# Optimization experiments

Hardware: AMD Instinct MI355X
Metric: run time of the kernel (lower is better)

## Reference

```python
import jax, jax.numpy as jnp
import numpy as np
from jax import lax

FEAT = 192   # features
GROUP = 3
B, H, W = 16, 64, 64
CIN = 2 * FEAT        # 384, input channels of x
CGATE = 4 * FEAT      # 768, gate channels


def _group_ids(C, g=GROUP):
    # contiguous channel blocks: channel c -> group c*g//C
    return (np.arange(C) * g) // C


def _mask_B(out_c, in_c, kw):
    # PixelRNN mask 'B' for a (1,kw) kernel: left-of-center columns fully
    # connected, center column obeys group rule (out_group >= in_group),
    # right-of-center columns blocked.
    og = _group_ids(out_c)[:, None]
    ig = _group_ids(in_c)[None, :]
    center = (og >= ig).astype(np.float32)  # (out_c, in_c)
    m = np.zeros((out_c, in_c, 1, kw), dtype=np.float32)
    m[:, :, :, : kw // 2] = 1.0
    m[:, :, 0, kw // 2] = center
    return jnp.asarray(m)


def _shuffle(h):
    # (B, 3*4*(F/3), H, W): group-major gate layout -> gate-major group layout
    b, c, hh, ww = h.shape
    return h.reshape(b, GROUP, 4, FEAT // GROUP, hh, ww) \
            .transpose(0, 2, 1, 3, 4, 5).reshape(b, c, hh, ww)


def setup_inputs() -> dict:
    key = jax.random.key(0)
    k1, k2, k3, k4, k5 = jax.random.split(key, 5)
    x = jax.random.normal(k1, (B, CIN, H, W), dtype=jnp.float32)
    w_i2s = jax.random.normal(k2, (CGATE, CIN, 1, 3), dtype=jnp.float32) * 0.02
    w_s2s = jax.random.normal(k3, (CGATE, FEAT, 1, 3), dtype=jnp.float32) * 0.02
    w_skip = jax.random.normal(k4, (CIN, FEAT, 1, 1), dtype=jnp.float32) * 0.05
    b_skip = jax.random.normal(k5, (CIN,), dtype=jnp.float32) * 0.01
    return {"x": x, "w_i2s": w_i2s, "w_s2s": w_s2s,
            "w_skip": w_skip, "b_skip": b_skip}


def reference(x, w_i2s, w_s2s, w_skip, b_skip):
    mask_i2s = _mask_B(CGATE, CIN, 3)
    mask_skip = _mask_B(CIN, FEAT, 1)

    # input-to-state: masked (1,3) conv, 'same' padding on width
    h = lax.conv_general_dilated(
        x, w_i2s * mask_i2s, (1, 1), ((0, 0), (1, 1)),
        dimension_numbers=("NCHW", "OIHW", "NCHW"))
    h = _shuffle(h)                       # (B, 4F, H, W)

    w1 = w_s2s[:, :, 0, :]                # (4F, F, 3) for 1D width conv
    h_rows = h.transpose(2, 0, 1, 3)      # (H, B, 4F, W)

    def step(carry, h_row):
        _h, c = carry                     # each (B, F, W)
        s = lax.conv_general_dilated(
            _h, w1, (1,), ((1, 1),),
            dimension_numbers=("NCW", "OIW", "NCW")) + h_row
        o, f, i, g = jnp.split(jax.nn.sigmoid(s), 4, axis=1)
        c = f * c + i * g
        _h = o * jnp.tanh(c)
        return (_h, c), _h

    init = (jnp.zeros((B, FEAT, W), x.dtype), jnp.zeros((B, FEAT, W), x.dtype))
    _, out_h = lax.scan(step, init, h_rows)   # (H, B, F, W)
    out_h = out_h.transpose(1, 2, 0, 3)       # (B, F, H, W)

    skip = lax.conv_general_dilated(
        out_h, w_skip * mask_skip, (1, 1), ((0, 0), (0, 0)),
        dimension_numbers=("NCHW", "OIHW", "NCHW")) + b_skip[None, :, None, None]
    return x + skip
```

## Files before the change

### kernel.cpp

```cpp
#include <hip/hip_runtime.h>
#include <hip/hip_cooperative_groups.h>
#include <cmath>

#define FEAT  192
#define CINCH 384
#define CGATE 768
#define BATCH 16
#define HH    64
#define WW    64
#define NP    (BATCH*HH*WW)
#define KI2S  768
#define KS2S  576
#define NBLK  192
#define SCANT 512

using bf16   = __bf16;
using bf16x8 = __attribute__((ext_vector_type(8))) __bf16;
using bf16x4 = __attribute__((ext_vector_type(4))) __bf16;
using f32x4  = __attribute__((ext_vector_type(4))) float;
typedef unsigned long long u64;

__device__ __forceinline__ void ic_store64(u64* p, u64 v) {
    __hip_atomic_store(p, v, __ATOMIC_RELAXED, __HIP_MEMORY_SCOPE_AGENT);
}
__device__ __forceinline__ u64 ic_load64(const u64* p) {
    return __hip_atomic_load(p, __ATOMIC_RELAXED, __HIP_MEMORY_SCOPE_AGENT);
}
__device__ __forceinline__ void ic_store32(unsigned* p, unsigned v) {
    __hip_atomic_store(p, v, __ATOMIC_RELAXED, __HIP_MEMORY_SCOPE_AGENT);
}
__device__ __forceinline__ unsigned ic_load32(const unsigned* p) {
    return __hip_atomic_load(p, __ATOMIC_RELAXED, __HIP_MEMORY_SCOPE_AGENT);
}
__device__ __forceinline__ void ic_store16(bf16* p, bf16 h) {
    union { bf16 h; unsigned short u; } cv; cv.h = h;
    __hip_atomic_store((unsigned short*)p, cv.u, __ATOMIC_RELAXED, __HIP_MEMORY_SCOPE_AGENT);
}
__device__ __forceinline__ float ic_load_bf16(const bf16* p) {
    union { unsigned short u; bf16 h; } cv;
    cv.u = __hip_atomic_load((const unsigned short*)p, __ATOMIC_RELAXED, __HIP_MEMORY_SCOPE_AGENT);
    return (float)cv.h;
}

__device__ __forceinline__ float sigm_fast(float v) {
    return __builtin_amdgcn_rcpf(1.f + __expf(-v));
}
__device__ __forceinline__ float tanh_fast(float v) {
    return 1.f - 2.f * __builtin_amdgcn_rcpf(1.f + __expf(2.f * v));
}

__global__ void pack_weights(const float* __restrict__ wi, const float* __restrict__ ws,
                             const float* __restrict__ wk,
                             bf16* __restrict__ WpA, bf16* __restrict__ WpS,
                             bf16* __restrict__ WpK, bf16* __restrict__ zp) {
    int tid = blockIdx.x * 256 + threadIdx.x;
    int stride = gridDim.x * 256;
    for (int idx = tid; idx < 512; idx += stride) zp[idx] = (bf16)0.f;
    for (int idx = tid; idx < CGATE * KI2S; idx += stride) {
        int cp = idx / KI2S, k = idx % KI2S;
        int q = cp / 192, r = cp % 192, g = r / 64, f = r % 64;
        int c = g * 256 + q * 64 + f;
        float v;
        if (k < CINCH) {
            v = wi[(c * CINCH + k) * 3 + 0];
        } else {
            int ic = k - CINCH;
            v = (g >= ic / 128) ? wi[(c * CINCH + ic) * 3 + 1] : 0.f;
        }
        WpA[idx] = (bf16)v;
    }
    for (int idx = tid; idx < CGATE * KS2S; idx += stride) {
        int oc = idx / KS2S, k = idx % KS2S;
        int t = k / FEAT, f = k % FEAT;
        WpS[idx] = (bf16)ws[(oc * FEAT + f) * 3 + t];
    }
    for (int idx = tid; idx < CINCH * FEAT; idx += stride) {
        int co = idx / FEAT, f = idx % FEAT;
        WpK[idx] = (co / 128 >= f / 64) ? (bf16)wk[idx] : (bf16)0.f;
    }
}

__global__ void pack_xc(const float* __restrict__ x, bf16* __restrict__ Xc) {
    __shared__ float tile[64][65];
    int b = blockIdx.x >> 6, y = blockIdx.x & 63;
    const float* xb = x + ((size_t)b * CINCH * HH + y) * WW;
    bf16* Xrow = Xc + (size_t)((b * HH + y) * WW) * CINCH;
    for (int ic0 = 0; ic0 < CINCH; ic0 += 64) {
        for (int rep = 0; rep < 16; ++rep) {
            int idx = rep * 256 + threadIdx.x;
            int i = idx >> 6, w = idx & 63;
            tile[i][w] = xb[(size_t)(ic0 + i) * (HH * WW) + w];
        }
        __syncthreads();
        for (int rep = 0; rep < 16; ++rep) {
            int idx = rep * 256 + threadIdx.x;
            int w = idx >> 6, i = idx & 63;
            Xrow[(size_t)w * CINCH + ic0 + i] = (bf16)tile[i][w];
        }
        __syncthreads();
    }
}

__global__ __launch_bounds__(SCANT, 2) void scan_kernel(
    const bf16* __restrict__ WpA,
    const bf16* __restrict__ Ws2s,
    const bf16* __restrict__ Wskip,
    const bf16* __restrict__ Xc,
    const bf16* __restrict__ zp,
    const float* __restrict__ x,
    const float* __restrict__ b_skip,
    float* __restrict__ out,
    bf16* __restrict__ hg,
    unsigned* __restrict__ cnt,
    bf16* __restrict__ Hring) {
    cooperative_groups::grid_group grid = cooperative_groups::this_grid();
    __shared__ __align__(16) bf16 hlds[66 * 200];
    __shared__ __align__(16) bf16 hnew[64 * 20];
    __shared__ __align__(16) bf16 As2[128 * 64];
    __shared__ __align__(16) bf16 Bs2[128 * 64];
    const int bid = blockIdx.x;
    const int b = (bid & 7) * 2 + (bid / 96);
    const int j = (bid >> 3) % 12;
    const int tid = threadIdx.x, lane = tid & 63, wid = tid >> 6;
    const int quad = lane >> 4, col = lane & 15;
    const int wh = wid & 3;
    const int wn = wid >> 2;
    const int mq = wid & 1, nq = wid >> 1;

    {
        const int total = 3 * 16 * 66 * 192 / 2;
        for (int i = bid * SCANT + tid; i < total; i += NBLK * SCANT)
            ((unsigned*)hg)[i] = 0u;
        if (tid < 32) cnt[(bid % 16) * 32 + tid] = 0u;
        if (tid >= 64 && tid < 96) cnt[512 + (bid % 16) * 32 + (tid - 64)] = 0u;
        for (int i = tid; i < 66 * 100; i += SCANT) ((unsigned*)hlds)[i] = 0u;
    }
    bf16x8 Ag[18];
    {
        int f = 16 * j + wh * 4 + (col >> 2), q = col & 3;
        const bf16* Arow = Ws2s + (size_t)(q * 192 + f) * KS2S + quad * 8;
        for (int kc = 0; kc < 18; ++kc) Ag[kc] = *(const bf16x8*)(Arow + kc * 32);
    }
    bf16x8 Ak[6];
    const int mtk = wid & 1, ntk = wid >> 1;
    {
        int co = 32 * j + mtk * 16 + col;
        const bf16* Krow = Wskip + (size_t)co * FEAT + quad * 8;
        for (int kc = 0; kc < 6; ++kc) Ak[kc] = *(const bf16x8*)(Krow + kc * 32);
    }
    const int fmine = 16 * j + wh * 4 + quad;
    const int lf = wh * 4 + quad;
    float cstate[2] = {0.f, 0.f};
    unsigned* myflags = cnt + b * 32;
    unsigned* gflags  = cnt + 512 + b * 32;
    grid.sync();

#define GSTAGE(M0, P0, K0) do {                                                    \
    _Pragma("unroll")                                                              \
    for (int r_ = 0; r_ < 2; ++r_) {                                               \
        int L_ = r_ * 512 + tid;                                                   \
        int row_ = L_ >> 3, slot_ = L_ & 7;                                        \
        int c_ = slot_ ^ (row_ & 7);                                               \
        const bf16* srcA = &WpA[(size_t)((M0) + row_) * KI2S + (K0) + c_ * 8];     \
        const bf16* srcB;                                                          \
        if ((K0) < 384) {                                                          \
            srcB = ((row_ & 63) == 0) ? (zp + c_ * 8)                              \
                 : &Xc[(size_t)((P0) + row_ - 1) * CINCH + (K0) + c_ * 8];         \
        } else {                                                                   \
            srcB = &Xc[(size_t)((P0) + row_) * CINCH + (K0) - 384 + c_ * 8];       \
        }                                                                          \
        bf16* dA = As2 + (size_t)(r_ * 512 + wid * 64) * 8;                        \
        bf16* dB = Bs2 + (size_t)(r_ * 512 + wid * 64) * 8;                        \
        __builtin_amdgcn_global_load_lds(                                          \
            (const __attribute__((address_space(1))) void*)srcA,                   \
            (__attribute__((address_space(3))) void*)dA, 16, 0, 0);                \
        __builtin_amdgcn_global_load_lds(                                          \
            (const __attribute__((address_space(1))) void*)srcB,                   \
            (__attribute__((address_space(3))) void*)dB, 16, 0, 0);                \
    }                                                                              \
} while (0)

#define GMFMA(ACC) do {                                                            \
    _Pragma("unroll")                                                              \
    for (int kk_ = 0; kk_ < 2; ++kk_) {                                            \
        bf16x8 af_[4], bv_[2];                                                     \
        _Pragma("unroll")                                                          \
        for (int mt_ = 0; mt_ < 4; ++mt_) {                                        \
            int row_ = mq * 64 + mt_ * 16 + col;                                   \
            int slot_ = (kk_ * 4 + quad) ^ (row_ & 7);                             \
            af_[mt_] = *(const bf16x8*)(&As2[row_ * 64 + slot_ * 8]);              \
        }                                                                          \
        _Pragma("unroll")                                                          \
        for (int nt_ = 0; nt_ < 2; ++nt_) {                                        \
            int row_ = nq * 32 + nt_ * 16 + col;                                   \
            int slot_ = (kk_ * 4 + quad) ^ (row_ & 7);                             \
            bv_[nt_] = *(const bf16x8*)(&Bs2[row_ * 64 + slot_ * 8]);              \
        }                                                                          \
        _Pragma("unroll")                                                          \
        for (int mt_ = 0; mt_ < 4; ++mt_)                                          \
            _Pragma("unroll")                                                      \
            for (int nt_ = 0; nt_ < 2; ++nt_)                                      \
                ACC[mt_][nt_] = __builtin_amdgcn_mfma_f32_16x16x32_bf16(           \
                    af_[mt_], bv_[nt_], ACC[mt_][nt_], 0, 0, 0);                   \
    }                                                                              \
} while (0)

#define GEPI(ACC, M0, YH) do {                                                     \
    _Pragma("unroll")                                                              \
    for (int mt_ = 0; mt_ < 4; ++mt_)                                              \
        _Pragma("unroll")                                                          \
        for (int nt_ = 0; nt_ < 2; ++nt_) {                                        \
            int m_ = (M0) + mq * 64 + mt_ * 16 + quad * 4;                         \
            int idx_ = nq * 32 + nt_ * 16 + col;                                   \
            int yy_ = (YH) * 2 + (idx_ >> 6), wl_ = idx_ & 63;                     \
            _Pragma("unroll")                                                      \
            for (int r_ = 0; r_ < 4; ++r_)                                         \
                ic_store16(&Hring[(((size_t)(m_ + r_) * 16 + b) * 8 +              \
                                   (yy_ & 7)) * 64 + wl_],                         \
                           (bf16)ACC[mt_][nt_][r_]);                               \
        }                                                                          \
} while (0)

#define HPREF(YY) do {                                                             \
    int slot_ = (YY) & 7;                                                          \
    _Pragma("unroll")                                                              \
    for (int i_ = 0; i_ < 2; ++i_) {                                               \
        int w_ = (wn * 2 + i_) * 16 + col;                                         \
        _Pragma("unroll")                                                          \
        for (int r_ = 0; r_ < 4; ++r_)                                             \
            hadd[i_][r_] = ic_load_bf16(&Hring[(((size_t)(r_ * FEAT + fmine) * 16  \
                                                 + b) * 8 + slot_) * 64 + w_]);    \
    }                                                                              \
} while (0)

    f32x4 accg[4][2];
    float hadd[2][4];

    {
        const int t0 = j;
        const int m0_ = (t0 % 6) * 128, yh_ = t0 / 6;
        const size_t p0_ = ((size_t)b * 64 + yh_ * 2) * 64;
        #pragma unroll
        for (int mt_ = 0; mt_ < 4; ++mt_)
            for (int nt_ = 0; nt_ < 2; ++nt_) accg[mt_][nt_] = f32x4{0.f, 0.f, 0.f, 0.f};
        for (int ki = 0; ki < 12; ++ki) {
            GSTAGE(m0_, p0_, ki * 64);
            __syncthreads();
            GMFMA(accg);
            __syncthreads();
        }
        GEPI(accg, m0_, yh_);
        __syncthreads();
        if (tid == 0) ic_store32(&gflags[j], 1u);
        while (true) {
            unsigned v = (lane < 12) ? ic_load32(&gflags[lane]) : 1u;
            if (__ballot(v >= 1u) == ~0ull) break;
            __builtin_amdgcn_s_sleep(1);
        }
        asm volatile("" ::: "memory");
        HPREF(0);
    }

    for (int y = 0; y < 64; ++y) {
        f32x4 acc[2] = {};
        for (int kc = 0; kc < 18; ++kc) {
            int k0 = kc * 32 + quad * 8;
            int t = k0 / FEAT, f = k0 % FEAT;
            #pragma unroll
            for (int i = 0; i < 2; ++i) {
                int w = (wn * 2 + i) * 16 + col;
                bf16x8 bfr = *(const bf16x8*)(&hlds[(w + t) * 200 + f]);
                acc[i] = __builtin_amdgcn_mfma_f32_16x16x32_bf16(Ag[kc], bfr, acc[i], 0, 0, 0);
            }
        }
        #pragma unroll
        for (int i = 0; i < 2; ++i) {
            int w = (wn * 2 + i) * 16 + col;
            float so = acc[i][0] + hadd[i][0];
            float sf = acc[i][1] + hadd[i][1];
            float si = acc[i][2] + hadd[i][2];
            float sg = acc[i][3] + hadd[i][3];
            float go = sigm_fast(so);
            float gf = sigm_fast(sf);
            float gi = sigm_fast(si);
            float gg = sigm_fast(sg);
            float cc = gf * cstate[i] + gi * gg;
            cstate[i] = cc;
            hnew[w * 20 + lf] = (bf16)(go * tanh_fast(cc));
        }
        __syncthreads();

        if (tid < 256) {
            bf16* dst = hg + ((size_t)(y % 3) * 16 + b) * (66 * 192);
            int w = tid >> 2, fo = (tid & 3) * 4;
            u64 v = *(const u64*)(&hnew[w * 20 + fo]);
            ic_store64((u64*)(dst + (size_t)(w + 1) * 192 + 16 * j + fo), v);
        }
        __syncthreads();
        if (tid == 0) ic_store32(&myflags[j], (unsigned)(y + 1));

        if (y < 60) {
            const int n_ = (y >> 2) + 1;
            const int t_ = j + 12 * n_;
            const int m0_ = (t_ % 6) * 128, yh_ = t_ / 6;
            const size_t p0_ = ((size_t)b * 64 + yh_ * 2) * 64;
            const int ph_ = y & 3;
            if (ph_ == 0) {
                #pragma unroll
                for (int mt_ = 0; mt_ < 4; ++mt_)
                    for (int nt_ = 0; nt_ < 2; ++nt_) accg[mt_][nt_] = f32x4{0.f, 0.f, 0.f, 0.f};
            }
            for (int ki = ph_ * 3; ki < ph_ * 3 + 3; ++ki) {
                GSTAGE(m0_, p0_, ki * 64);
                __syncthreads();
                GMFMA(accg);
                __syncthreads();
            }
            if (ph_ == 3) {
                GEPI(accg, m0_, yh_);
                __syncthreads();
                if (tid == 0) ic_store32(&gflags[j], (unsigned)(n_ + 1));
            }
        }

        if (y < 63) {
            const int yhreq = (y + 1) >> 1;
            unsigned tgt = 0;
            if (lane < 12) {
                int o = (lane >= 6) ? 1 : 0;
                tgt = (yhreq >= o) ? (unsigned)(((yhreq - o) >> 1) + 1) : 0u;
            }
            while (true) {
                unsigned v = (lane < 12) ? ic_load32(&gflags[lane]) : 0u;
                if (__ballot(v >= tgt) == ~0ull) break;
                __builtin_amdgcn_s_sleep(1);
            }
            asm volatile("" ::: "memory");
            HPREF(y + 1);
        }

        if (y > 0) {
            const int ym = y - 1;
            f32x4 acc2 = {};
            int wsk = ntk * 16 + col;
            for (int kc = 0; kc < 6; ++kc) {
                bf16x8 bfr = *(const bf16x8*)(&hlds[(wsk + 1) * 200 + kc * 32 + quad * 8]);
                acc2 = __builtin_amdgcn_mfma_f32_16x16x32_bf16(Ak[kc], bfr, acc2, 0, 0, 0);
            }
            for (int r = 0; r < 4; ++r) {
                int co = 32 * j + mtk * 16 + quad * 4 + r;
                size_t xi = ((size_t)(b * CINCH + co) * HH + ym) * WW + wsk;
                out[xi] = x[xi] + b_skip[co] + acc2[r];
            }
        }
        __syncthreads();

        {
            const unsigned tgt = (unsigned)(y + 1);
            while (true) {
                unsigned v = (lane < 12) ? ic_load32(&myflags[lane]) : tgt;
                if (__ballot(v >= tgt) == ~0ull) break;
                __builtin_amdgcn_s_sleep(1);
            }
            asm volatile("" ::: "memory");
        }

        {
            const u64* src = (const u64*)(hg + ((size_t)(y % 3) * 16 + b) * (66 * 192));
            #pragma unroll
            for (int it = 0; it < 7; ++it) {
                int c = it * SCANT + tid;
                if (c < 66 * 48) {
                    u64 v = ic_load64(src + c);
                    int w = c / 48, fc = c % 48;
                    *(u64*)(&hlds[w * 200 + fc * 4]) = v;
                }
            }
        }
        __syncthreads();
    }

    {
        f32x4 acc2 = {};
        int wsk = ntk * 16 + col;
        for (int kc = 0; kc < 6; ++kc) {
            bf16x8 bfr = *(const bf16x8*)(&hlds[(wsk + 1) * 200 + kc * 32 + quad * 8]);
            acc2 = __builtin_amdgcn_mfma_f32_16x16x32_bf16(Ak[kc], bfr, acc2, 0, 0, 0);
        }
        for (int r = 0; r < 4; ++r) {
            int co = 32 * j + mtk * 16 + quad * 4 + r;
            size_t xi = ((size_t)(b * CINCH + co) * HH + 63) * WW + wsk;
            out[xi] = x[xi] + b_skip[co] + acc2[r];
        }
    }

#undef GSTAGE
#undef GMFMA
#undef GEPI
#undef HPREF
}

extern "C" void kernel_launch(void* const* d_in, const int* in_sizes, int n_in,
                              void* d_out, int out_size, void* d_ws, size_t ws_size,
                              hipStream_t stream) {
    const float* x      = (const float*)d_in[0];
    const float* w_i2s  = (const float*)d_in[1];
    const float* w_s2s  = (const float*)d_in[2];
    const float* w_skip = (const float*)d_in[3];
    const float* b_skip = (const float*)d_in[4];
    float* out = (float*)d_out;

    char* ws = (char*)d_ws;
    bf16* Xc    = (bf16*)ws;
    size_t off  = (size_t)NP * CINCH * 2;
    bf16* WpA   = (bf16*)(ws + off); off += (size_t)CGATE * KI2S * 2;
    bf16* WpS   = (bf16*)(ws + off); off += (size_t)CGATE * KS2S * 2;
    bf16* WpK   = (bf16*)(ws + off); off += (size_t)CINCH * FEAT * 2;
    bf16* hg    = (bf16*)(ws + off); off += (size_t)3 * 16 * 66 * 192 * 2;
    bf16* Hring = (bf16*)(ws + off); off += (size_t)CGATE * 16 * 8 * 64 * 2;
    unsigned* cnt = (unsigned*)(ws + off); off += 4096;
    bf16* zp    = (bf16*)(ws + off); off += 1024;

    pack_weights<<<256, 256, 0, stream>>>(w_i2s, w_s2s, w_skip, WpA, WpS, WpK, zp);
    pack_xc<<<BATCH * HH, 256, 0, stream>>>(x, Xc);

    void* args[] = { (void*)&WpA, (void*)&WpS, (void*)&WpK, (void*)&Xc, (void*)&zp,
                     (void*)&x, (void*)&b_skip, (void*)&out, (void*)&hg, (void*)&cnt,
                     (void*)&Hring };
    hipLaunchCooperativeKernel((const void*)scan_kernel, dim3(NBLK), dim3(SCANT),
                               args, 0, stream);
}
```

Before: 771.7 us.

## Offload input-to-state GEMM to dedicated producer blocks with deeper ring buffer

Adds 64 producer blocks to the cooperative grid. They compute the input-to-state gate GEMM tiles ahead of the recurrent scan, using double-buffered LDS staging, and write the results into a Hring buffer enlarged from 8 to 16 rows. The 192 scan blocks no longer interleave GEMM slices into each recurrence step, which takes that work off the latency-critical scan loop. In exchange the grid needs more co-resident blocks and more LDS per block, and producers must spin on scan progress flags to avoid overrunning the ring.

```diff
diff --git a/kernel.cpp b/kernel.cpp
--- a/kernel.cpp
+++ b/kernel.cpp
@@ -11,8 +11,11 @@
 #define NP    (BATCH*HH*WW)
 #define KI2S  768
 #define KS2S  576
-#define NBLK  192
+#define NSCAN 192
+#define NPROD 64
+#define NBLK  (NSCAN+NPROD)
 #define SCANT 512
+#define RING  16
 
 using bf16   = __bf16;
 using bf16x8 = __attribute__((ext_vector_type(8))) __bf16;
@@ -114,48 +117,29 @@
     unsigned* __restrict__ cnt,
     bf16* __restrict__ Hring) {
     cooperative_groups::grid_group grid = cooperative_groups::this_grid();
-    __shared__ __align__(16) bf16 hlds[66 * 200];
-    __shared__ __align__(16) bf16 hnew[64 * 20];
-    __shared__ __align__(16) bf16 As2[128 * 64];
-    __shared__ __align__(16) bf16 Bs2[128 * 64];
+    __shared__ __align__(16) bf16 smem[32768];
+    bf16* const hlds = smem;
+    bf16* const hnew = smem + 13200;
     const int bid = blockIdx.x;
-    const int b = (bid & 7) * 2 + (bid / 96);
-    const int j = (bid >> 3) % 12;
+    const bool isScan = bid < NSCAN;
     const int tid = threadIdx.x, lane = tid & 63, wid = tid >> 6;
     const int quad = lane >> 4, col = lane & 15;
-    const int wh = wid & 3;
-    const int wn = wid >> 2;
     const int mq = wid & 1, nq = wid >> 1;
 
     {
         const int total = 3 * 16 * 66 * 192 / 2;
         for (int i = bid * SCANT + tid; i < total; i += NBLK * SCANT)
             ((unsigned*)hg)[i] = 0u;
-        if (tid < 32) cnt[(bid % 16) * 32 + tid] = 0u;
-        if (tid >= 64 && tid < 96) cnt[512 + (bid % 16) * 32 + (tid - 64)] = 0u;
-        for (int i = tid; i < 66 * 100; i += SCANT) ((unsigned*)hlds)[i] = 0u;
-    }
-    bf16x8 Ag[18];
-    {
-        int f = 16 * j + wh * 4 + (col >> 2), q = col & 3;
-        const bf16* Arow = Ws2s + (size_t)(q * 192 + f) * KS2S + quad * 8;
-        for (int kc = 0; kc < 18; ++kc) Ag[kc] = *(const bf16x8*)(Arow + kc * 32);
-    }
-    bf16x8 Ak[6];
-    const int mtk = wid & 1, ntk = wid >> 1;
-    {
-        int co = 32 * j + mtk * 16 + col;
-        const bf16* Krow = Wskip + (size_t)co * FEAT + quad * 8;
-        for (int kc = 0; kc < 6; ++kc) Ak[kc] = *(const bf16x8*)(Krow + kc * 32);
-    }
-    const int fmine = 16 * j + wh * 4 + quad;
-    const int lf = wh * 4 + quad;
-    float cstate[2] = {0.f, 0.f};
-    unsigned* myflags = cnt + b * 32;
-    unsigned* gflags  = cnt + 512 + b * 32;
+        if (isScan) {
+            if (tid < 32) cnt[(bid % 16) * 32 + tid] = 0u;
+            if (tid >= 64 && tid < 96) cnt[512 + (bid % 16) * 32 + (tid - 64)] = 0u;
+        }
+    }
     grid.sync();
 
-#define GSTAGE(M0, P0, K0) do {                                                    \
+#define GSTAGE(BUF, M0, P0, K0) do {                                               \
+    bf16* const dAb_ = smem + (BUF) * 8192;                                        \
+    bf16* const dBb_ = smem + 16384 + (BUF) * 8192;                                \
     _Pragma("unroll")                                                              \
     for (int r_ = 0; r_ < 2; ++r_) {                                               \
         int L_ = r_ * 512 + tid;                                                   \
@@ -169,18 +153,20 @@
         } else {                                                                   \
             srcB = &Xc[(size_t)((P0) + row_) * CINCH + (K0) - 384 + c_ * 8];       \
         }                                                                          \
-        bf16* dA = As2 + (size_t)(r_ * 512 + wid * 64) * 8;                        \
-        bf16* dB = Bs2 + (size_t)(r_ * 512 + wid * 64) * 8;                        \
         __builtin_amdgcn_global_load_lds(                                          \
             (const __attribute__((address_space(1))) void*)srcA,                   \
-            (__attribute__((address_space(3))) void*)dA, 16, 0, 0);                \
+            (__attribute__((address_space(3))) void*)(dAb_ + (size_t)(r_ * 512 +   \
+                wid * 64) * 8), 16, 0, 0);                                         \
         __builtin_amdgcn_global_load_lds(                                          \
             (const __attribute__((address_space(1))) void*)srcB,                   \
-            (__attribute__((address_space(3))) void*)dB, 16, 0, 0);                \
+            (__attribute__((address_space(3))) void*)(dBb_ + (size_t)(r_ * 512 +   \
+                wid * 64) * 8), 16, 0, 0);                                         \
     }                                                                              \
 } while (0)
 
-#define GMFMA(ACC) do {                                                            \
+#define GMFMA(ACC, BUF) do {                                                       \
+    const bf16* const sAb_ = smem + (BUF) * 8192;                                  \
+    const bf16* const sBb_ = smem + 16384 + (BUF) * 8192;                          \
     _Pragma("unroll")                                                              \
     for (int kk_ = 0; kk_ < 2; ++kk_) {                                            \
         bf16x8 af_[4], bv_[2];                                                     \
@@ -188,13 +174,13 @@
         for (int mt_ = 0; mt_ < 4; ++mt_) {                                        \
             int row_ = mq * 64 + mt_ * 16 + col;                                   \
             int slot_ = (kk_ * 4 + quad) ^ (row_ & 7);                             \
-            af_[mt_] = *(const bf16x8*)(&As2[row_ * 64 + slot_ * 8]);              \
+            af_[mt_] = *(const bf16x8*)(&sAb_[row_ * 64 + slot_ * 8]);             \
         }                                                                          \
         _Pragma("unroll")                                                          \
         for (int nt_ = 0; nt_ < 2; ++nt_) {                                        \
             int row_ = nq * 32 + nt_ * 16 + col;                                   \
             int slot_ = (kk_ * 4 + quad) ^ (row_ & 7);                             \
-            bv_[nt_] = *(const bf16x8*)(&Bs2[row_ * 64 + slot_ * 8]);              \
+            bv_[nt_] = *(const bf16x8*)(&sBb_[row_ * 64 + slot_ * 8]);             \
         }                                                                          \
         _Pragma("unroll")                                                          \
         for (int mt_ = 0; mt_ < 4; ++mt_)                                          \
@@ -205,7 +191,7 @@
     }                                                                              \
 } while (0)
 
-#define GEPI(ACC, M0, YH) do {                                                     \
+#define GEPI(ACC, M0, YH, BB) do {                                                 \
     _Pragma("unroll")                                                              \
     for (int mt_ = 0; mt_ < 4; ++mt_)                                              \
         _Pragma("unroll")                                                          \
@@ -215,43 +201,102 @@
             int yy_ = (YH) * 2 + (idx_ >> 6), wl_ = idx_ & 63;                     \
             _Pragma("unroll")                                                      \
             for (int r_ = 0; r_ < 4; ++r_)                                         \
-                ic_store16(&Hring[(((size_t)(m_ + r_) * 16 + b) * 8 +              \
-                                   (yy_ & 7)) * 64 + wl_],                         \
+                ic_store16(&Hring[(((size_t)(m_ + r_) * 16 + (BB)) * RING +        \
+                                   (yy_ & (RING - 1))) * 64 + wl_],                \
                            (bf16)ACC[mt_][nt_][r_]);                               \
         }                                                                          \
 } while (0)
 
 #define HPREF(YY) do {                                                             \
-    int slot_ = (YY) & 7;                                                          \
+    int slot_ = (YY) & (RING - 1);                                                 \
     _Pragma("unroll")                                                              \
     for (int i_ = 0; i_ < 2; ++i_) {                                               \
         int w_ = (wn * 2 + i_) * 16 + col;                                         \
         _Pragma("unroll")                                                          \
         for (int r_ = 0; r_ < 4; ++r_)                                             \
             hadd[i_][r_] = ic_load_bf16(&Hring[(((size_t)(r_ * FEAT + fmine) * 16  \
-                                                 + b) * 8 + slot_) * 64 + w_]);    \
+                                                 + b) * RING + slot_) * 64 + w_]); \
     }                                                                              \
 } while (0)
 
-    f32x4 accg[4][2];
+    if (!isScan) {
+        const int pid = bid - NSCAN;
+        const int pb = pid & 15;
+        const int pslot = pid >> 4;
+        unsigned* phf = cnt + pb * 32;
+        unsigned* pgf = cnt + 512 + pb * 32;
+        for (int n = 0; n < 16; ++n) {
+            for (int q3 = 0; q3 < 3; ++q3) {
+                const int jj = pslot + q3 * 4;
+                const int t_ = jj + 12 * n;
+                const int m0_ = (t_ % 6) * 128, yh_ = t_ / 6;
+                const size_t p0_ = ((size_t)pb * 64 + yh_ * 2) * 64;
+                const int needi = 2 * yh_ - (RING - 2);
+                if (needi > 0) {
+                    const unsigned need = (unsigned)needi;
+                    while (true) {
+                        unsigned v = (lane < 12) ? ic_load32(&phf[lane]) : need;
+                        if (__ballot(v >= need) == ~0ull) break;
+                        __builtin_amdgcn_s_sleep(8);
+                    }
+                    asm volatile("" ::: "memory");
+                }
+                f32x4 accg[4][2];
+                #pragma unroll
+                for (int mt_ = 0; mt_ < 4; ++mt_)
+                    for (int nt_ = 0; nt_ < 2; ++nt_)
+                        accg[mt_][nt_] = f32x4{0.f, 0.f, 0.f, 0.f};
+                GSTAGE(0, m0_, p0_, 0);
+                #pragma unroll 1
+                for (int ki = 0; ki < 12; ++ki) {
+                    if (ki < 11) {
+                        GSTAGE((ki + 1) & 1, m0_, p0_, (ki + 1) * 64);
+                        asm volatile("s_waitcnt vmcnt(4)" ::: "memory");
+                    } else {
+                        asm volatile("s_waitcnt vmcnt(0)" ::: "memory");
+                    }
+                    __builtin_amdgcn_sched_barrier(0);
+                    __builtin_amdgcn_s_barrier();
+                    GMFMA(accg, ki & 1);
+                    asm volatile("s_waitcnt lgkmcnt(0)" ::: "memory");
+                    __builtin_amdgcn_sched_barrier(0);
+                    __builtin_amdgcn_s_barrier();
+                }
+                GEPI(accg, m0_, yh_, pb);
+                __syncthreads();
+                if (tid == 0) ic_store32(&pgf[jj], (unsigned)(n + 1));
+            }
+        }
+        return;
+    }
+
+    const int b = (bid & 7) * 2 + (bid / 96);
+    const int j = (bid >> 3) % 12;
+    const int wh = wid & 3;
+    const int wn = wid >> 2;
+    bf16x8 Ag[18];
+    {
+        int f = 16 * j + wh * 4 + (col >> 2), q = col & 3;
+        const bf16* Arow = Ws2s + (size_t)(q * 192 + f) * KS2S + quad * 8;
+        for (int kc = 0; kc < 18; ++kc) Ag[kc] = *(const bf16x8*)(Arow + kc * 32);
+    }
+    bf16x8 Ak[6];
+    const int mtk = wid & 1, ntk = wid >> 1;
+    {
+        int co = 32 * j + mtk * 16 + col;
+        const bf16* Krow = Wskip + (size_t)co * FEAT + quad * 8;
+        for (int kc = 0; kc < 6; ++kc) Ak[kc] = *(const bf16x8*)(Krow + kc * 32);
+    }
+    const int fmine = 16 * j + wh * 4 + quad;
+    const int lf = wh * 4 + quad;
+    float cstate[2] = {0.f, 0.f};
     float hadd[2][4];
+    unsigned* hflags = cnt + b * 32;
+    unsigned* gflags = cnt + 512 + b * 32;
+    for (int i = tid; i < 66 * 100; i += SCANT) ((unsigned*)hlds)[i] = 0u;
+    __syncthreads();
 
     {
-        const int t0 = j;
-        const int m0_ = (t0 % 6) * 128, yh_ = t0 / 6;
-        const size_t p0_ = ((size_t)b * 64 + yh_ * 2) * 64;
-        #pragma unroll
-        for (int mt_ = 0; mt_ < 4; ++mt_)
-            for (int nt_ = 0; nt_ < 2; ++nt_) accg[mt_][nt_] = f32x4{0.f, 0.f, 0.f, 0.f};
-        for (int ki = 0; ki < 12; ++ki) {
-            GSTAGE(m0_, p0_, ki * 64);
-            __syncthreads();
-            GMFMA(accg);
-            __syncthreads();
-        }
-        GEPI(accg, m0_, yh_);
-        __syncthreads();
-        if (tid == 0) ic_store32(&gflags[j], 1u);
         while (true) {
             unsigned v = (lane < 12) ? ic_load32(&gflags[lane]) : 1u;
             if (__ballot(v >= 1u) == ~0ull) break;
@@ -297,31 +342,7 @@
             ic_store64((u64*)(dst + (size_t)(w + 1) * 192 + 16 * j + fo), v);
         }
         __syncthreads();
-        if (tid == 0) ic_store32(&myflags[j], (unsigned)(y + 1));
-
-        if (y < 60) {
-            const int n_ = (y >> 2) + 1;
-            const int t_ = j + 12 * n_;
-            const int m0_ = (t_ % 6) * 128, yh_ = t_ / 6;
-            const size_t p0_ = ((size_t)b * 64 + yh_ * 2) * 64;
-            const int ph_ = y & 3;
-            if (ph_ == 0) {
-                #pragma unroll
-                for (int mt_ = 0; mt_ < 4; ++mt_)
-                    for (int nt_ = 0; nt_ < 2; ++nt_) accg[mt_][nt_] = f32x4{0.f, 0.f, 0.f, 0.f};
-            }
-            for (int ki = ph_ * 3; ki < ph_ * 3 + 3; ++ki) {
-                GSTAGE(m0_, p0_, ki * 64);
-                __syncthreads();
-                GMFMA(accg);
-                __syncthreads();
-            }
-            if (ph_ == 3) {
-                GEPI(accg, m0_, yh_);
-                __syncthreads();
-                if (tid == 0) ic_store32(&gflags[j], (unsigned)(n_ + 1));
-            }
-        }
+        if (tid == 0) ic_store32(&hflags[j], (unsigned)(y + 1));
 
         if (y < 63) {
             const int yhreq = (y + 1) >> 1;
@@ -358,7 +379,7 @@
         {
             const unsigned tgt = (unsigned)(y + 1);
             while (true) {
-                unsigned v = (lane < 12) ? ic_load32(&myflags[lane]) : tgt;
+                unsigned v = (lane < 12) ? ic_load32(&hflags[lane]) : tgt;
                 if (__ballot(v >= tgt) == ~0ull) break;
                 __builtin_amdgcn_s_sleep(1);
             }
@@ -417,7 +438,7 @@
     bf16* WpS   = (bf16*)(ws + off); off += (size_t)CGATE * KS2S * 2;
     bf16* WpK   = (bf16*)(ws + off); off += (size_t)CINCH * FEAT * 2;
     bf16* hg    = (bf16*)(ws + off); off += (size_t)3 * 16 * 66 * 192 * 2;
-    bf16* Hring = (bf16*)(ws + off); off += (size_t)CGATE * 16 * 8 * 64 * 2;
+    bf16* Hring = (bf16*)(ws + off); off += (size_t)CGATE * 16 * RING * 64 * 2;
     unsigned* cnt = (unsigned*)(ws + off); off += 4096;
     bf16* zp    = (bf16*)(ws + off); off += 1024;
 
```

Result: faster. 749.0 us (-3.0%).
